# Kernel optimization log

Measured on AMD Instinct MI355X. Metric: run time of the kernel, lower is better.

## Reference

```python
import jax, jax.numpy as jnp
import numpy as np

D_MODEL = 768
NUM_HEADS = 12
HEAD_DIM = D_MODEL // NUM_HEADS
WINDOW_SIZE = 512
TOP_K = 64
SCALE = 1.0 / np.sqrt(HEAD_DIM).astype(np.float32)
NEG_INF = float('-inf')


def setup_inputs() -> dict:
    key = jax.random.key(0)
    ks = jax.random.split(key, 12)
    B, S, D = 2, 2048, D_MODEL
    std = 1.0 / np.sqrt(D)
    return {
        'query': jax.random.normal(ks[0], (B, S, D), jnp.float32),
        'key':   jax.random.normal(ks[1], (B, S, D), jnp.float32),
        'value': jax.random.normal(ks[2], (B, S, D), jnp.float32),
        'Wq': jax.random.normal(ks[3], (D, D), jnp.float32) * std,
        'bq': jnp.zeros((D,), jnp.float32),
        'Wk': jax.random.normal(ks[4], (D, D), jnp.float32) * std,
        'bk': jnp.zeros((D,), jnp.float32),
        'Wv': jax.random.normal(ks[5], (D, D), jnp.float32) * std,
        'bv': jnp.zeros((D,), jnp.float32),
        'Wo': jax.random.normal(ks[6], (D, D), jnp.float32) * std,
        'bo': jnp.zeros((D,), jnp.float32),
    }


def _split_heads(x, B, S):
    # [B,S,D] -> [B,H,S,hd]
    return x.reshape(B, S, NUM_HEADS, HEAD_DIM).transpose(0, 2, 1, 3)


def _forward(query, key, value, Wq, bq, Wk, bk, Wv, bv, Wo, bo):
    B, S, D = query.shape
    q = _split_heads(query @ Wq.T + bq, B, S)
    k = _split_heads(key @ Wk.T + bk, B, S)
    v = _split_heads(value @ Wv.T + bv, B, S)

    # dense scores [B,H,S,S]
    scores = jnp.einsum('bhqd,bhkd->bhqk', q, k) * SCALE

    # --- windowed (causal local) branch ---
    i = jnp.arange(S)[:, None]
    j = jnp.arange(S)[None, :]
    # window mask intersected with causal tril: i - ws//2 <= j <= i
    wmask = (j >= i - WINDOW_SIZE // 2) & (j <= i)  # [S,S]
    w_scores = jnp.where(wmask[None, None], scores, NEG_INF)
    w_probs = jax.nn.softmax(w_scores, axis=-1)
    ctx_w = jnp.einsum('bhqk,bhkd->bhqd', w_probs, v)

    # --- sparse top-k branch ---
    tk_vals, tk_idx = jax.lax.top_k(scores, TOP_K)  # [B,H,S,TOP_K]
    sparse = jnp.full_like(scores, NEG_INF)
    bi = jnp.arange(B)[:, None, None, None]
    hi = jnp.arange(NUM_HEADS)[None, :, None, None]
    si = jnp.arange(S)[None, None, :, None]
    sparse = sparse.at[bi, hi, si, tk_idx].set(tk_vals)
    s_probs = jax.nn.softmax(sparse, axis=-1)
    ctx_s = jnp.einsum('bhqk,bhkd->bhqd', s_probs, v)

    combined = (ctx_w + ctx_s) * 0.5  # [B,H,S,hd]
    combined = combined.transpose(0, 2, 1, 3).reshape(B, S, D)
    return combined @ Wo.T + bo


def reference(query, key, value, Wq, bq, Wk, bk, Wv, bv, Wo, bo):
    return _forward(query, key, value, Wq, bq, Wk, bk, Wv, bv, Wo, bo)
```

## Files before the change

### kernel.cpp

```cpp
#include <hip/hip_runtime.h>
#include <hip/hip_fp16.h>
#include <stdint.h>
#include <math.h>

#define NH    12
#define SEQ   2048
#define BATCH 2
#define DM    768
#define HD    64
#define SCALEF 0.125f

typedef unsigned short u16;
typedef unsigned int   u32;
typedef unsigned long long u64;
typedef __attribute__((ext_vector_type(8))) short bf16x8;
typedef __attribute__((ext_vector_type(8))) _Float16 h16x8;
typedef __attribute__((ext_vector_type(4))) float f32x4;

__device__ __forceinline__ u16 f2bf(float f){
  u32 u = __float_as_uint(f);
  u32 r = u + 0x7fffu + ((u >> 16) & 1u);
  return (u16)(r >> 16);
}
__device__ __forceinline__ float bf2f(u16 x){ return __uint_as_float(((u32)x) << 16); }
__device__ __forceinline__ u16 f2h(float f){ return __half_as_ushort(__float2half(f)); }
__device__ __forceinline__ float h2f(u16 x){ return __half2float(__ushort_as_half(x)); }

__device__ __forceinline__ int dpp_sumi(int x){
  x += __builtin_amdgcn_update_dpp(0, x, 0x111, 0xf, 0xf, true);
  x += __builtin_amdgcn_update_dpp(0, x, 0x112, 0xf, 0xf, true);
  x += __builtin_amdgcn_update_dpp(0, x, 0x114, 0xf, 0xf, true);
  x += __builtin_amdgcn_update_dpp(0, x, 0x118, 0xf, 0xf, true);
  x += __builtin_amdgcn_update_dpp(0, x, 0x142, 0xa, 0xf, true);
  x += __builtin_amdgcn_update_dpp(0, x, 0x143, 0xc, 0xf, true);
  return __builtin_amdgcn_readlane(x, 63);
}
__device__ __forceinline__ int dpp_scan_incl(int x){
  x += __builtin_amdgcn_update_dpp(0, x, 0x111, 0xf, 0xf, true);
  x += __builtin_amdgcn_update_dpp(0, x, 0x112, 0xf, 0xf, true);
  x += __builtin_amdgcn_update_dpp(0, x, 0x114, 0xf, 0xf, true);
  x += __builtin_amdgcn_update_dpp(0, x, 0x118, 0xf, 0xf, true);
  x += __builtin_amdgcn_update_dpp(0, x, 0x142, 0xa, 0xf, true);
  x += __builtin_amdgcn_update_dpp(0, x, 0x143, 0xc, 0xf, true);
  return x;
}
__device__ __forceinline__ float dpp_sumf(float x){
  #define ASTEP(ctrl, rm) x += __int_as_float(__builtin_amdgcn_update_dpp(0, __float_as_int(x), ctrl, rm, 0xf, true));
  ASTEP(0x111,0xf) ASTEP(0x112,0xf) ASTEP(0x114,0xf) ASTEP(0x118,0xf) ASTEP(0x142,0xa) ASTEP(0x143,0xc)
  #undef ASTEP
  return __uint_as_float((u32)__builtin_amdgcn_readlane(__float_as_int(x), 63));
}
__device__ __forceinline__ float dpp_maxf(float x){
  #define MSTEP(ctrl, rm) { int o = __float_as_int(x); \
    x = fmaxf(x, __int_as_float(__builtin_amdgcn_update_dpp(o, o, ctrl, rm, 0xf, false))); }
  MSTEP(0x111,0xf) MSTEP(0x112,0xf) MSTEP(0x114,0xf) MSTEP(0x118,0xf) MSTEP(0x142,0xa) MSTEP(0x143,0xc)
  #undef MSTEP
  return __uint_as_float((u32)__builtin_amdgcn_readlane(__float_as_int(x), 63));
}

__device__ __forceinline__ int pb_off(int q, int k){
  return (q << 11) + ((((k >> 3) ^ (q & 7)) << 3) | (k & 7));
}
__device__ __forceinline__ int ps_off(int kc, int q, int d){
  return (kc << 10) + (q << 6) + ((((d >> 2) ^ q) & 15) << 2) + (d & 3);
}

__global__ void cvt_kernel(const float* s0, const float* s1, const float* s2, const float* s3,
                           u16* d0, u16* d1, u16* d2, u16* d3, int n){
  const float* s; u16* d;
  switch (blockIdx.y){
    case 0: s = s0; d = d0; break;
    case 1: s = s1; d = d1; break;
    case 2: s = s2; d = d2; break;
    default: s = s3; d = d3; break;
  }
  int i = (blockIdx.x * 256 + threadIdx.x) * 4;
  if (i < n){
    float4 v = *(const float4*)(s + i);
    ushort4 o;
    o.x = f2bf(v.x); o.y = f2bf(v.y); o.z = f2bf(v.z); o.w = f2bf(v.w);
    *(ushort4*)(d + i) = o;
  }
}

template<int MODE>
__global__ __launch_bounds__(256) void gemm_bt(const u16* __restrict__ Aall, const u16* __restrict__ Wall,
      const float* __restrict__ bz0, const float* __restrict__ bz1, const float* __restrict__ bz2,
      u16* __restrict__ outb, float* __restrict__ outf){
  __shared__ u16 As[128][40];
  __shared__ u16 Bs[128][40];
  const int zz = blockIdx.z;
  const u16* A = Aall + (size_t)zz * 4096 * 768;
  const u16* W = Wall + (size_t)zz * 768 * 768;
  const float* bias = (zz == 0) ? bz0 : (zz == 1 ? bz1 : bz2);
  const int m0 = blockIdx.x * 128, n0 = blockIdx.y * 128;
  const int t = threadIdx.x, lane = t & 63, wv = t >> 6;
  const int wm = wv >> 1, wn = wv & 1;
  f32x4 acc[4][4] = {};
  const int arow = t >> 1, aseg = t & 1;
  const u16* ap = A + (size_t)(m0 + arow) * 768 + aseg * 16;
  const u16* bp = W + (size_t)(n0 + arow) * 768 + aseg * 16;
  for (int kt = 0; kt < 768; kt += 32){
    uint4 av0 = *(const uint4*)(ap + kt);
    uint4 av1 = *(const uint4*)(ap + kt + 8);
    uint4 bv0 = *(const uint4*)(bp + kt);
    uint4 bv1 = *(const uint4*)(bp + kt + 8);
    __syncthreads();
    *(uint4*)&As[arow][aseg*16]     = av0;
    *(uint4*)&As[arow][aseg*16 + 8] = av1;
    *(uint4*)&Bs[arow][aseg*16]     = bv0;
    *(uint4*)&Bs[arow][aseg*16 + 8] = bv1;
    __syncthreads();
    bf16x8 af[4], bq[4];
    #pragma unroll
    for (int i = 0; i < 4; ++i) af[i] = *(const bf16x8*)&As[wm*64 + i*16 + (lane & 15)][(lane >> 4) * 8];
    #pragma unroll
    for (int i = 0; i < 4; ++i) bq[i] = *(const bf16x8*)&Bs[wn*64 + i*16 + (lane & 15)][(lane >> 4) * 8];
    #pragma unroll
    for (int mi = 0; mi < 4; ++mi)
      #pragma unroll
      for (int ni = 0; ni < 4; ++ni)
        acc[mi][ni] = __builtin_amdgcn_mfma_f32_16x16x32_bf16(af[mi], bq[ni], acc[mi][ni], 0, 0, 0);
  }
  #pragma unroll
  for (int mi = 0; mi < 4; ++mi){
    #pragma unroll
    for (int ni = 0; ni < 4; ++ni){
      const int n = n0 + wn*64 + ni*16 + (lane & 15);
      const float bval = bias[n];
      const int mbase = m0 + wm*64 + mi*16 + (lane >> 4) * 4;
      if (MODE == 0 && zz == 2){
        const int bb = mbase >> 11, ss = mbase & 2047;
        const int hh = n >> 6, dd = n & 63;
        u64 pk = 0;
        #pragma unroll
        for (int r = 0; r < 4; ++r) pk |= (u64)f2h(acc[mi][ni][r] + bval) << (16 * r);
        *(u64*)(outb + (size_t)2 * 3145728 + (((size_t)(bb * NH + hh) * HD + dd) * SEQ + ss)) = pk;
      } else if (MODE == 0){
        #pragma unroll
        for (int r = 0; r < 4; ++r){
          const int m = mbase + r;
          const int bb = m >> 11, ss = m & 2047, hh = n >> 6, dd = n & 63;
          outb[(size_t)zz * 3145728 + (((size_t)bb * NH + hh) * SEQ + ss) * HD + dd] = f2bf(acc[mi][ni][r] + bval);
        }
      } else {
        #pragma unroll
        for (int r = 0; r < 4; ++r){
          const int m = mbase + r;
          outf[(size_t)m * DM + n] = acc[mi][ni][r] + bval;
        }
      }
    }
  }
}

__global__ __launch_bounds__(1024, 8) void attn5_kernel(const u16* __restrict__ Qh,
      const u16* __restrict__ Kh, const u16* __restrict__ Vt, u16* __restrict__ ctxb){
  __shared__ __align__(16) u32 smem[20480];
  u16*  Pm    = (u16*)smem;
  float* psum = (float*)(smem + 16384);
  float* s_val = (float*)(smem + 16384);
  u32*  s_idx  = (u32*)(smem + 16384 + 1024);

  const int q0 = blockIdx.x * 16;
  const int h = blockIdx.y, b = blockIdx.z, bh = b * NH + h;
  const int t = threadIdx.x, lane = t & 63, w = t >> 6;
  const u16* Qb  = Qh + ((size_t)bh * SEQ + q0) * HD;
  const u16* Kb  = Kh + (size_t)bh * SEQ * HD;
  const u16* Vtb = Vt + (size_t)bh * HD * SEQ;

  {
    const int qcol = lane & 15;
    const bf16x8 qa0 = *(const bf16x8*)(Qb + qcol * HD + (lane >> 4) * 8);
    const bf16x8 qa1 = *(const bf16x8*)(Qb + qcol * HD + 32 + (lane >> 4) * 8);
    #pragma unroll 4
    for (int tile = 0; tile < 8; ++tile){
      const int kr = w * 128 + tile * 16 + (lane & 15);
      const bf16x8 ka0 = *(const bf16x8*)(Kb + (size_t)kr * HD + (lane >> 4) * 8);
      const bf16x8 ka1 = *(const bf16x8*)(Kb + (size_t)kr * HD + 32 + (lane >> 4) * 8);
      f32x4 d = {};
      d = __builtin_amdgcn_mfma_f32_16x16x32_bf16(ka0, qa0, d, 0, 0, 0);
      d = __builtin_amdgcn_mfma_f32_16x16x32_bf16(ka1, qa1, d, 0, 0, 0);
      const int kbase = w * 128 + tile * 16 + (lane >> 4) * 4;
      const u32 lo = (u32)f2h(d[0] * SCALEF) | ((u32)f2h(d[1] * SCALEF) << 16);
      const u32 hi = (u32)f2h(d[2] * SCALEF) | ((u32)f2h(d[3] * SCALEF) << 16);
      const int off = (qcol << 10) | ((kbase >> 1) ^ (qcol << 1));
      *(u64*)(smem + off) = (u64)lo | ((u64)hi << 32);
    }
  }
  __syncthreads();

  const int qi = q0 + w;
  const int sw = w << 1;
  u32* rowp = smem + (w << 10);
  u32 ukp[16]; float wvv[5];
  #pragma unroll
  for (int i = 0; i < 16; ++i){
    const u32 dw = rowp[(lane + 64 * i) ^ sw];
    const u32 s = (dw >> 15) & 0x00010001u;
    ukp[i] = dw ^ (0x80008000u | (s * 0x7fffu));
  }
  const int start = (qi - 256 > 0) ? (qi - 256) : 0;
  #pragma unroll
  for (int it = 0; it < 5; ++it){
    const int c0 = start + lane + it * 64;
    const int c = (c0 <= qi) ? c0 : qi;
    const u32 dw = rowp[(c >> 1) ^ sw];
    const u16 hb = (c & 1) ? (u16)(dw >> 16) : (u16)(dw & 0xffffu);
    wvv[it] = (c0 <= qi) ? h2f(hb) : -INFINITY;
  }
  __asm__ volatile("" ::: "memory");

  {
    float* svals = s_val + w * 64;
    u32*  sidx   = s_idx + w * 64;

    u32 tval = 0;
    for (int bit = 15; bit >= 0; --bit){
      const u32 cand = tval | (1u << bit);
      int c = 0;
      #pragma unroll
      for (int i = 0; i < 16; ++i){
        c += ((ukp[i] & 0xffffu) >= cand) ? 1 : 0;
        c += ((ukp[i] >> 16) >= cand) ? 1 : 0;
      }
      c = dpp_sumi(c);
      if (c >= 64){ tval = cand; if (c == 64) break; }
    }
    int ngt = 0;
    #pragma unroll
    for (int i = 0; i < 16; ++i){
      ngt += ((ukp[i] & 0xffffu) > tval) ? 1 : 0;
      ngt += ((ukp[i] >> 16) > tval) ? 1 : 0;
    }
    const int pre = dpp_scan_incl(ngt) - ngt;
    const int G = dpp_sumi(ngt);
    const int r_need = 64 - G;
    int k2 = 0;
    #pragma unroll
    for (int i = 0; i < 16; ++i){
      #pragma unroll
      for (int hh = 0; hh < 2; ++hh){
        const u32 kk = hh ? (ukp[i] >> 16) : (ukp[i] & 0xffffu);
        if (kk > tval){
          const u16 hb = (kk & 0x8000u) ? (u16)(kk & 0x7fffu) : (u16)(~kk & 0xffffu);
          svals[pre + k2] = h2f(hb);
          sidx[pre + k2] = 2 * lane + 128 * i + hh;
          ++k2;
        }
      }
    }
    {
      const u16 thb = (tval & 0x8000u) ? (u16)(tval & 0x7fffu) : (u16)(~tval & 0xffffu);
      const float tv = h2f(thb);
      int filled = 0;
      for (int i = 0; i < 16 && filled < r_need; ++i){
        #pragma unroll
        for (int hh = 0; hh < 2; ++hh){
          const u32 kk = hh ? (ukp[i] >> 16) : (ukp[i] & 0xffffu);
          const bool eq = (kk == tval);
          const u64 bal = __ballot(eq);
          const int myrank = filled + (int)__popcll(bal & ((1ull << lane) - 1ull));
          if (eq && myrank < r_need){
            svals[G + myrank] = tv;
            sidx[G + myrank] = 2 * lane + 128 * i + hh;
          }
          filled += (int)__popcll(bal);
        }
      }
    }
    __asm__ volatile("" ::: "memory");

    const float svv = svals[lane];
    const float m1 = dpp_maxf(svv);
    const float e1 = __expf(svv - m1);
    const float Z1 = dpp_sumf(e1);
    const float padd = e1 * (0.5f / Z1);
    const int  ksp  = (int)sidx[lane];

    float wm = -INFINITY;
    #pragma unroll
    for (int it = 0; it < 5; ++it) wm = fmaxf(wm, wvv[it]);
    wm = dpp_maxf(wm);
    float zs = 0.f;
    #pragma unroll
    for (int it = 0; it < 5; ++it){
      const int c = start + lane + it * 64;
      if (c <= qi){ const float e = __expf(wvv[it] - wm); wvv[it] = e; zs += e; }
    }
    zs = dpp_sumf(zs);
    const float inv = 0.5f / zs;

    {
      uint4* prow = (uint4*)(Pm + (w << 11));
      const uint4 z4 = {0u, 0u, 0u, 0u};
      #pragma unroll
      for (int i = 0; i < 4; ++i) prow[lane + i * 64] = z4;
      __asm__ volatile("" ::: "memory");
      #pragma unroll
      for (int it = 0; it < 5; ++it){
        const int c = start + lane + it * 64;
        if (c <= qi) Pm[pb_off(w, c)] = f2h(wvv[it] * inv);
      }
      __asm__ volatile("" ::: "memory");
      u16* cell = &Pm[pb_off(w, ksp)];
      *cell = f2h(h2f(*cell) + padd);
    }
  }
  __syncthreads();

  {
    const int kc = w >> 2, mi = w & 3;
    f32x4 acc = {};
    #pragma unroll 4
    for (int ks = 0; ks < 16; ++ks){
      const int kk = kc * 512 + ks * 32;
      const h16x8 va = *(const h16x8*)(Vtb + (size_t)(mi * 16 + (lane & 15)) * SEQ + kk + (lane >> 4) * 8);
      const h16x8 pf = *(const h16x8*)&Pm[pb_off(lane & 15, kk + (lane >> 4) * 8)];
      acc = __builtin_amdgcn_mfma_f32_16x16x32_f16(va, pf, acc, 0, 0, 0);
    }
    const int q = lane & 15, dbase = mi * 16 + (lane >> 4) * 4;
    *(f32x4*)&psum[ps_off(kc, q, dbase)] = acc;
  }
  __syncthreads();

  {
    const int q = t >> 6, d = t & 63;
    const float r = psum[ps_off(0, q, d)] + psum[ps_off(1, q, d)]
                  + psum[ps_off(2, q, d)] + psum[ps_off(3, q, d)];
    ctxb[((size_t)(b * SEQ + q0 + q)) * DM + h * HD + d] = f2bf(r);
  }
}

extern "C" void kernel_launch(void* const* d_in, const int* in_sizes, int n_in,
                              void* d_out, int out_size, void* d_ws, size_t ws_size,
                              hipStream_t stream){
  const float* q_in = (const float*)d_in[0];
  const float* k_in = (const float*)d_in[1];
  const float* v_in = (const float*)d_in[2];
  const float* Wq = (const float*)d_in[3];
  const float* bq = (const float*)d_in[4];
  const float* Wk = (const float*)d_in[5];
  const float* bk = (const float*)d_in[6];
  const float* Wv = (const float*)d_in[7];
  const float* bv = (const float*)d_in[8];
  const float* Wo = (const float*)d_in[9];
  const float* bo = (const float*)d_in[10];

  char* ws = (char*)d_ws;
  u16* Xb   = (u16*)ws;
  u16* Wb   = (u16*)(ws + 18874368);
  u16* QKVh = (u16*)(ws + 23592960);
  u16* ctxb = (u16*)(ws + 42467328);

  cvt_kernel<<<dim3(3145728 / 1024, 3), 256, 0, stream>>>(
      q_in, k_in, v_in, nullptr, Xb, Xb + 3145728, Xb + 2 * 3145728, nullptr, 3145728);
  cvt_kernel<<<dim3(589824 / 1024, 4), 256, 0, stream>>>(
      Wq, Wk, Wv, Wo, Wb, Wb + 589824, Wb + 2 * 589824, Wb + 3 * 589824, 589824);

  gemm_bt<0><<<dim3(32, 6, 3), 256, 0, stream>>>(Xb, Wb, bq, bk, bv, QKVh, nullptr);

  attn5_kernel<<<dim3(SEQ / 16, NH, BATCH), 1024, 0, stream>>>(
      QKVh, QKVh + 3145728, QKVh + 2 * 3145728, ctxb);

  gemm_bt<1><<<dim3(32, 6, 1), 256, 0, stream>>>(
      ctxb, Wb + 3 * 589824, bo, bo, bo, nullptr, (float*)d_out);
}
```

Measured before the change: 319.5 us.

## Replace bitwise top-k threshold search with two-pass LDS radix histogram select

```diff
diff --git a/kernel.cpp b/kernel.cpp
--- a/kernel.cpp
+++ b/kernel.cpp
@@ -154,13 +154,11 @@
   }
 }
 
-__global__ __launch_bounds__(1024, 8) void attn5_kernel(const u16* __restrict__ Qh,
+__global__ __launch_bounds__(1024, 8) void attn6_kernel(const u16* __restrict__ Qh,
       const u16* __restrict__ Kh, const u16* __restrict__ Vt, u16* __restrict__ ctxb){
   __shared__ __align__(16) u32 smem[20480];
   u16*  Pm    = (u16*)smem;
   float* psum = (float*)(smem + 16384);
-  float* s_val = (float*)(smem + 16384);
-  u32*  s_idx  = (u32*)(smem + 16384 + 1024);
 
   const int q0 = blockIdx.x * 16;
   const int h = blockIdx.y, b = blockIdx.z, bh = b * NH + h;
@@ -193,40 +191,77 @@
   const int qi = q0 + w;
   const int sw = w << 1;
   u32* rowp = smem + (w << 10);
-  u32 ukp[16]; float wvv[5];
+  u32* hw   = smem + 16384 + (w << 8);
+  u32 ukp[16];
   #pragma unroll
   for (int i = 0; i < 16; ++i){
     const u32 dw = rowp[(lane + 64 * i) ^ sw];
     const u32 s = (dw >> 15) & 0x00010001u;
     ukp[i] = dw ^ (0x80008000u | (s * 0x7fffu));
   }
-  const int start = (qi - 256 > 0) ? (qi - 256) : 0;
-  #pragma unroll
-  for (int it = 0; it < 5; ++it){
-    const int c0 = start + lane + it * 64;
-    const int c = (c0 <= qi) ? c0 : qi;
-    const u32 dw = rowp[(c >> 1) ^ sw];
-    const u16 hb = (c & 1) ? (u16)(dw >> 16) : (u16)(dw & 0xffffu);
-    wvv[it] = (c0 <= qi) ? h2f(hb) : -INFINITY;
-  }
   __asm__ volatile("" ::: "memory");
 
-  {
-    float* svals = s_val + w * 64;
-    u32*  sidx   = s_idx + w * 64;
-
-    u32 tval = 0;
-    for (int bit = 15; bit >= 0; --bit){
-      const u32 cand = tval | (1u << bit);
-      int c = 0;
-      #pragma unroll
-      for (int i = 0; i < 16; ++i){
-        c += ((ukp[i] & 0xffffu) >= cand) ? 1 : 0;
-        c += ((ukp[i] >> 16) >= cand) ? 1 : 0;
-      }
-      c = dpp_sumi(c);
-      if (c >= 64){ tval = cand; if (c == 64) break; }
-    }
+  int tb, G_byte;
+  const uint4 z4 = {0u, 0u, 0u, 0u};
+  {
+    *(uint4*)&hw[lane << 2] = z4;
+    __asm__ volatile("s_waitcnt lgkmcnt(0)" ::: "memory");
+    #pragma unroll
+    for (int i = 0; i < 16; ++i){
+      atomicAdd(&hw[(ukp[i] >> 8) & 0xffu], 1u);
+      atomicAdd(&hw[ukp[i] >> 24], 1u);
+    }
+    __asm__ volatile("s_waitcnt lgkmcnt(0)" ::: "memory");
+    const uint4 hv = *(const uint4*)&hw[lane << 2];
+    const int s_l = (int)(hv.x + hv.y + hv.z + hv.w);
+    const int incl = dpp_scan_incl(s_l);
+    const int ab3 = 2048 - incl;
+    const int ab2 = ab3 + (int)hv.w;
+    const int ab1 = ab2 + (int)hv.z;
+    const int ab0 = ab1 + (int)hv.y;
+    int pk = 0;
+    if      (ab3 < 64 && ab3 + (int)hv.w >= 64) pk = ((((lane << 2) + 3) << 16) | ab3);
+    else if (ab2 < 64 && ab2 + (int)hv.z >= 64) pk = ((((lane << 2) + 2) << 16) | ab2);
+    else if (ab1 < 64 && ab1 + (int)hv.y >= 64) pk = ((((lane << 2) + 1) << 16) | ab1);
+    else if (ab0 < 64 && ab0 + (int)hv.x >= 64) pk = ((((lane << 2) + 0) << 16) | ab0);
+    const int win = dpp_sumi(pk);
+    tb = win >> 16; G_byte = win & 0xffff;
+  }
+  u32 tval; int G, r_need;
+  {
+    *(uint4*)&hw[lane << 2] = z4;
+    __asm__ volatile("s_waitcnt lgkmcnt(0)" ::: "memory");
+    #pragma unroll
+    for (int i = 0; i < 16; ++i){
+      const u32 lo = ukp[i] & 0xffffu;
+      const u32 hi = ukp[i] >> 16;
+      if ((int)(lo >> 8) == tb) atomicAdd(&hw[lo & 0xffu], 1u);
+      if ((int)(hi >> 8) == tb) atomicAdd(&hw[hi & 0xffu], 1u);
+    }
+    __asm__ volatile("s_waitcnt lgkmcnt(0)" ::: "memory");
+    const uint4 hv = *(const uint4*)&hw[lane << 2];
+    const int s_l = (int)(hv.x + hv.y + hv.z + hv.w);
+    const int incl = dpp_scan_incl(s_l);
+    const int tot2 = __builtin_amdgcn_readlane(incl, 63);
+    const int ab3 = G_byte + tot2 - incl;
+    const int ab2 = ab3 + (int)hv.w;
+    const int ab1 = ab2 + (int)hv.z;
+    const int ab0 = ab1 + (int)hv.y;
+    int pk = 0;
+    if      (ab3 < 64 && ab3 + (int)hv.w >= 64) pk = ((((lane << 2) + 3) << 16) | ab3);
+    else if (ab2 < 64 && ab2 + (int)hv.z >= 64) pk = ((((lane << 2) + 2) << 16) | ab2);
+    else if (ab1 < 64 && ab1 + (int)hv.y >= 64) pk = ((((lane << 2) + 1) << 16) | ab1);
+    else if (ab0 < 64 && ab0 + (int)hv.x >= 64) pk = ((((lane << 2) + 0) << 16) | ab0);
+    const int win = dpp_sumi(pk);
+    const int lb = win >> 16;
+    G = win & 0xffff;
+    tval = (u32)((tb << 8) | lb);
+    r_need = 64 - G;
+  }
+
+  {
+    float* svals = (float*)hw;
+    u32*  sidx   = hw + 64;
     int ngt = 0;
     #pragma unroll
     for (int i = 0; i < 16; ++i){
@@ -234,8 +269,6 @@
       ngt += ((ukp[i] >> 16) > tval) ? 1 : 0;
     }
     const int pre = dpp_scan_incl(ngt) - ngt;
-    const int G = dpp_sumi(ngt);
-    const int r_need = 64 - G;
     int k2 = 0;
     #pragma unroll
     for (int i = 0; i < 16; ++i){
@@ -278,6 +311,16 @@
     const float padd = e1 * (0.5f / Z1);
     const int  ksp  = (int)sidx[lane];
 
+    const int start = (qi - 256 > 0) ? (qi - 256) : 0;
+    float wvv[5];
+    #pragma unroll
+    for (int it = 0; it < 5; ++it){
+      const int c0 = start + lane + it * 64;
+      const int c = (c0 <= qi) ? c0 : qi;
+      const u32 dw = rowp[(c >> 1) ^ sw];
+      const u16 hb = (c & 1) ? (u16)(dw >> 16) : (u16)(dw & 0xffffu);
+      wvv[it] = (c0 <= qi) ? h2f(hb) : -INFINITY;
+    }
     float wm = -INFINITY;
     #pragma unroll
     for (int it = 0; it < 5; ++it) wm = fmaxf(wm, wvv[it]);
@@ -293,7 +336,6 @@
 
     {
       uint4* prow = (uint4*)(Pm + (w << 11));
-      const uint4 z4 = {0u, 0u, 0u, 0u};
       #pragma unroll
       for (int i = 0; i < 4; ++i) prow[lane + i * 64] = z4;
       __asm__ volatile("" ::: "memory");
@@ -360,7 +402,7 @@
 
   gemm_bt<0><<<dim3(32, 6, 3), 256, 0, stream>>>(Xb, Wb, bq, bk, bv, QKVh, nullptr);
 
-  attn5_kernel<<<dim3(SEQ / 16, NH, BATCH), 1024, 0, stream>>>(
+  attn6_kernel<<<dim3(SEQ / 16, NH, BATCH), 1024, 0, stream>>>(
       QKVh, QKVh + 3145728, QKVh + 2 * 3145728, ctxb);
 
   gemm_bt<1><<<dim3(32, 6, 1), 256, 0, stream>>>(
```

Measured after the change: 313.5 us. About the same (-1.9%).

## Replace bitwise radix top-k with max-anchored bisection and LDS candidate compaction

Applied to the files above, without the earlier changes.

```diff
diff --git a/kernel.cpp b/kernel.cpp
--- a/kernel.cpp
+++ b/kernel.cpp
@@ -25,6 +25,11 @@
 __device__ __forceinline__ float bf2f(u16 x){ return __uint_as_float(((u32)x) << 16); }
 __device__ __forceinline__ u16 f2h(float f){ return __half_as_ushort(__float2half(f)); }
 __device__ __forceinline__ float h2f(u16 x){ return __half2float(__ushort_as_half(x)); }
+
+__device__ __forceinline__ float kval(u32 k){
+  const u16 hb = (k & 0x8000u) ? (u16)(k & 0x7fffu) : (u16)(~k & 0xffffu);
+  return h2f(hb);
+}
 
 __device__ __forceinline__ int dpp_sumi(int x){
   x += __builtin_amdgcn_update_dpp(0, x, 0x111, 0xf, 0xf, true);
@@ -56,6 +61,13 @@
   MSTEP(0x111,0xf) MSTEP(0x112,0xf) MSTEP(0x114,0xf) MSTEP(0x118,0xf) MSTEP(0x142,0xa) MSTEP(0x143,0xc)
   #undef MSTEP
   return __uint_as_float((u32)__builtin_amdgcn_readlane(__float_as_int(x), 63));
+}
+__device__ __forceinline__ int dpp_maxi(int x){
+  #define ISTEP(ctrl, rm) { int o = x; int y = __builtin_amdgcn_update_dpp(o, o, ctrl, rm, 0xf, false); \
+    x = (x > y) ? x : y; }
+  ISTEP(0x111,0xf) ISTEP(0x112,0xf) ISTEP(0x114,0xf) ISTEP(0x118,0xf) ISTEP(0x142,0xa) ISTEP(0x143,0xc)
+  #undef ISTEP
+  return __builtin_amdgcn_readlane(x, 63);
 }
 
 __device__ __forceinline__ int pb_off(int q, int k){
@@ -154,13 +166,11 @@
   }
 }
 
-__global__ __launch_bounds__(1024, 8) void attn5_kernel(const u16* __restrict__ Qh,
+__global__ __launch_bounds__(1024, 8) void attn7_kernel(const u16* __restrict__ Qh,
       const u16* __restrict__ Kh, const u16* __restrict__ Vt, u16* __restrict__ ctxb){
   __shared__ __align__(16) u32 smem[20480];
   u16*  Pm    = (u16*)smem;
   float* psum = (float*)(smem + 16384);
-  float* s_val = (float*)(smem + 16384);
-  u32*  s_idx  = (u32*)(smem + 16384 + 1024);
 
   const int q0 = blockIdx.x * 16;
   const int h = blockIdx.y, b = blockIdx.z, bh = b * NH + h;
@@ -193,14 +203,113 @@
   const int qi = q0 + w;
   const int sw = w << 1;
   u32* rowp = smem + (w << 10);
-  u32 ukp[16]; float wvv[5];
+  u32* cand = smem + 16384 + (w << 8);
+  u32 ukp[16];
   #pragma unroll
   for (int i = 0; i < 16; ++i){
     const u32 dw = rowp[(lane + 64 * i) ^ sw];
     const u32 s = (dw >> 15) & 0x00010001u;
     ukp[i] = dw ^ (0x80008000u | (s * 0x7fffu));
   }
+  __asm__ volatile("" ::: "memory");
+
+  u32 pmx = ukp[0];
+  #pragma unroll
+  for (int i = 1; i < 16; ++i){
+    const u32 a = ukp[i];
+    const u32 l = (a & 0xffffu) > (pmx & 0xffffu) ? (a & 0xffffu) : (pmx & 0xffffu);
+    const u32 hh = (a >> 16) > (pmx >> 16) ? (a >> 16) : (pmx >> 16);
+    pmx = l | (hh << 16);
+  }
+  u32 Mk = (pmx & 0xffffu) > (pmx >> 16) ? (pmx & 0xffffu) : (pmx >> 16);
+  Mk = (u32)dpp_maxi((int)Mk);
+  const float m1 = kval(Mk);
+
+  u32 blo = 0;  int c_lo = 2048;
+  u32 bhi = Mk + 1; int c_hi = 0;
+  {
+    u32 tm = (Mk > 1024u) ? (Mk - 1024u) : 1u;
+    if (tm >= bhi) tm = (blo + bhi) >> 1;
+    #pragma unroll 1
+    for (int it = 0; it < 12; ++it){
+      int cl = 0;
+      #pragma unroll
+      for (int i = 0; i < 16; ++i){
+        cl += ((ukp[i] & 0xffffu) >= tm) ? 1 : 0;
+        cl += ((ukp[i] >> 16) >= tm) ? 1 : 0;
+      }
+      const int c = dpp_sumi(cl);
+      if (c >= 64){ blo = tm; c_lo = c; if (c <= 240) break; }
+      else        { bhi = tm; c_hi = c; }
+      const u32 nt = (blo + bhi) >> 1;
+      if (nt == blo) break;
+      tm = nt;
+    }
+  }
+
+  int n_c;
+  {
+    int cl = 0;
+    #pragma unroll
+    for (int i = 0; i < 16; ++i){
+      cl += ((ukp[i] & 0xffffu) >= blo) ? 1 : 0;
+      cl += ((ukp[i] >> 16) >= blo) ? 1 : 0;
+    }
+    const int incl = dpp_scan_incl(cl);
+    const int totalc = __builtin_amdgcn_readlane(incl, 63);
+    int pos = incl - cl;
+    #pragma unroll
+    for (int i = 0; i < 16; ++i){
+      #pragma unroll
+      for (int hh = 0; hh < 2; ++hh){
+        const u32 kk = hh ? (ukp[i] >> 16) : (ukp[i] & 0xffffu);
+        if (kk >= blo && pos < 256){
+          const int idx = 2 * lane + (i << 7) + hh;
+          cand[pos] = (kk << 16) | (u32)(2047 - idx);
+          ++pos;
+        }
+      }
+    }
+    n_c = totalc < 256 ? totalc : 256;
+  }
+  __asm__ volatile("s_waitcnt lgkmcnt(0)" ::: "memory");
+
+  u32 cj[4];
+  #pragma unroll
+  for (int j = 0; j < 4; ++j){
+    const int s = lane + 64 * j;
+    const u32 vv = cand[s];
+    cj[j] = (s < n_c) ? vv : 0u;
+  }
+  while (bhi - blo > 1u){
+    const u32 tm = (blo + bhi) >> 1;
+    const u32 kthr = tm << 16;
+    int cl = 0;
+    #pragma unroll
+    for (int j = 0; j < 4; ++j) cl += (cj[j] >= kthr) ? 1 : 0;
+    const int c = dpp_sumi(cl);
+    if (c >= 64){ blo = tm; c_lo = c; } else { bhi = tm; c_hi = c; }
+  }
+  const u32 T = blo;
+  const int G = c_hi;
+  const int r_need = 64 - G;
+
+  float ev[4]; int eqc = 0;
+  float zl = 0.f;
+  #pragma unroll
+  for (int j = 0; j < 4; ++j){
+    const u32 key = cj[j] >> 16;
+    ev[j] = __expf(kval(key) - m1);
+    zl += (key > T) ? ev[j] : 0.f;
+    eqc += (key == T) ? 1 : 0;
+  }
+  const int pre_eq = dpp_scan_incl(eqc) - eqc;
+  const float eT = __expf(kval(T) - m1);
+  const float Z1 = dpp_sumf(zl) + (float)r_need * eT;
+  const float inv1 = 0.5f / Z1;
+
   const int start = (qi - 256 > 0) ? (qi - 256) : 0;
+  float wvv[5];
   #pragma unroll
   for (int it = 0; it < 5; ++it){
     const int c0 = start + lane + it * 64;
@@ -209,102 +318,44 @@
     const u16 hb = (c & 1) ? (u16)(dw >> 16) : (u16)(dw & 0xffffu);
     wvv[it] = (c0 <= qi) ? h2f(hb) : -INFINITY;
   }
-  __asm__ volatile("" ::: "memory");
-
-  {
-    float* svals = s_val + w * 64;
-    u32*  sidx   = s_idx + w * 64;
-
-    u32 tval = 0;
-    for (int bit = 15; bit >= 0; --bit){
-      const u32 cand = tval | (1u << bit);
-      int c = 0;
-      #pragma unroll
-      for (int i = 0; i < 16; ++i){
-        c += ((ukp[i] & 0xffffu) >= cand) ? 1 : 0;
-        c += ((ukp[i] >> 16) >= cand) ? 1 : 0;
-      }
-      c = dpp_sumi(c);
-      if (c >= 64){ tval = cand; if (c == 64) break; }
-    }
-    int ngt = 0;
-    #pragma unroll
-    for (int i = 0; i < 16; ++i){
-      ngt += ((ukp[i] & 0xffffu) > tval) ? 1 : 0;
-      ngt += ((ukp[i] >> 16) > tval) ? 1 : 0;
-    }
-    const int pre = dpp_scan_incl(ngt) - ngt;
-    const int G = dpp_sumi(ngt);
-    const int r_need = 64 - G;
-    int k2 = 0;
-    #pragma unroll
-    for (int i = 0; i < 16; ++i){
-      #pragma unroll
-      for (int hh = 0; hh < 2; ++hh){
-        const u32 kk = hh ? (ukp[i] >> 16) : (ukp[i] & 0xffffu);
-        if (kk > tval){
-          const u16 hb = (kk & 0x8000u) ? (u16)(kk & 0x7fffu) : (u16)(~kk & 0xffffu);
-          svals[pre + k2] = h2f(hb);
-          sidx[pre + k2] = 2 * lane + 128 * i + hh;
-          ++k2;
-        }
-      }
-    }
-    {
-      const u16 thb = (tval & 0x8000u) ? (u16)(tval & 0x7fffu) : (u16)(~tval & 0xffffu);
-      const float tv = h2f(thb);
-      int filled = 0;
-      for (int i = 0; i < 16 && filled < r_need; ++i){
-        #pragma unroll
-        for (int hh = 0; hh < 2; ++hh){
-          const u32 kk = hh ? (ukp[i] >> 16) : (ukp[i] & 0xffffu);
-          const bool eq = (kk == tval);
-          const u64 bal = __ballot(eq);
-          const int myrank = filled + (int)__popcll(bal & ((1ull << lane) - 1ull));
-          if (eq && myrank < r_need){
-            svals[G + myrank] = tv;
-            sidx[G + myrank] = 2 * lane + 128 * i + hh;
-          }
-          filled += (int)__popcll(bal);
-        }
-      }
-    }
+  float wm = -INFINITY;
+  #pragma unroll
+  for (int it = 0; it < 5; ++it) wm = fmaxf(wm, wvv[it]);
+  wm = dpp_maxf(wm);
+  float zs = 0.f;
+  #pragma unroll
+  for (int it = 0; it < 5; ++it){
+    const int c = start + lane + it * 64;
+    if (c <= qi){ const float e = __expf(wvv[it] - wm); wvv[it] = e; zs += e; }
+  }
+  zs = dpp_sumf(zs);
+  const float inv = 0.5f / zs;
+
+  {
+    uint4* prow = (uint4*)(Pm + (w << 11));
+    const uint4 z4 = {0u, 0u, 0u, 0u};
+    #pragma unroll
+    for (int i = 0; i < 4; ++i) prow[lane + i * 64] = z4;
     __asm__ volatile("" ::: "memory");
-
-    const float svv = svals[lane];
-    const float m1 = dpp_maxf(svv);
-    const float e1 = __expf(svv - m1);
-    const float Z1 = dpp_sumf(e1);
-    const float padd = e1 * (0.5f / Z1);
-    const int  ksp  = (int)sidx[lane];
-
-    float wm = -INFINITY;
-    #pragma unroll
-    for (int it = 0; it < 5; ++it) wm = fmaxf(wm, wvv[it]);
-    wm = dpp_maxf(wm);
-    float zs = 0.f;
     #pragma unroll
     for (int it = 0; it < 5; ++it){
       const int c = start + lane + it * 64;
-      if (c <= qi){ const float e = __expf(wvv[it] - wm); wvv[it] = e; zs += e; }
-    }
-    zs = dpp_sumf(zs);
-    const float inv = 0.5f / zs;
-
-    {
-      uint4* prow = (uint4*)(Pm + (w << 11));
-      const uint4 z4 = {0u, 0u, 0u, 0u};
-      #pragma unroll
-      for (int i = 0; i < 4; ++i) prow[lane + i * 64] = z4;
-      __asm__ volatile("" ::: "memory");
-      #pragma unroll
-      for (int it = 0; it < 5; ++it){
-        const int c = start + lane + it * 64;
-        if (c <= qi) Pm[pb_off(w, c)] = f2h(wvv[it] * inv);
+      if (c <= qi) Pm[pb_off(w, c)] = f2h(wvv[it] * inv);
+    }
+    __asm__ volatile("" ::: "memory");
+    int rloc = pre_eq;
+    #pragma unroll
+    for (int j = 0; j < 4; ++j){
+      const u32 key = cj[j] >> 16;
+      const bool isgt = key > T;
+      const bool iseq = (key == T);
+      const bool sel = isgt || (iseq && rloc < r_need);
+      if (iseq) ++rloc;
+      if (sel){
+        const int idx = 2047 - (int)(cj[j] & 0x7ffu);
+        u16* cell = &Pm[pb_off(w, idx)];
+        *cell = f2h(h2f(*cell) + ev[j] * inv1);
       }
-      __asm__ volatile("" ::: "memory");
-      u16* cell = &Pm[pb_off(w, ksp)];
-      *cell = f2h(h2f(*cell) + padd);
     }
   }
   __syncthreads();
@@ -360,7 +411,7 @@
 
   gemm_bt<0><<<dim3(32, 6, 3), 256, 0, stream>>>(Xb, Wb, bq, bk, bv, QKVh, nullptr);
 
-  attn5_kernel<<<dim3(SEQ / 16, NH, BATCH), 1024, 0, stream>>>(
+  attn7_kernel<<<dim3(SEQ / 16, NH, BATCH), 1024, 0, stream>>>(
       QKVh, QKVh + 3145728, QKVh + 2 * 3145728, ctxb);
 
   gemm_bt<1><<<dim3(32, 6, 1), 256, 0, stream>>>(
```

Result: faster. 305.5 us (-4.4%).
